# Kernel optimization log

Measured on AMD Instinct MI355X. Metric: run time of the kernel, lower is better.

## Reference

```python
import jax, jax.numpy as jnp
import numpy as np
from jax import lax

B, S, N, DIM = 4, 512, 16, 8
D_MODEL, D_STATE = 1024, 64
INPUT_SIZE = N * DIM
LN_EPS = 1e-5


def setup_inputs() -> dict:
    key = jax.random.key(0)
    ks = jax.random.split(key, 8)
    s = 0.02
    x = jax.random.normal(ks[0], (B, S, N, DIM), dtype=jnp.float32)
    W_emb = jax.random.normal(ks[1], (INPUT_SIZE, D_MODEL), dtype=jnp.float32) * s
    b_emb = jnp.zeros((D_MODEL,), jnp.float32)
    W_xp = jax.random.normal(ks[2], (D_MODEL, 2 * D_STATE + 1), dtype=jnp.float32) * s
    b_xp = jnp.zeros((2 * D_STATE + 1,), jnp.float32)
    # A init: -exp(arange(1, d_state+1) * 0.1), matching the torch module
    A = -jnp.exp(jnp.arange(1, D_STATE + 1, dtype=jnp.float32) * 0.1)
    Dp = jnp.ones((D_MODEL,), jnp.float32)
    gamma = jnp.ones((D_MODEL,), jnp.float32)
    beta = jnp.zeros((D_MODEL,), jnp.float32)
    W_out = jax.random.normal(ks[3], (D_MODEL, INPUT_SIZE), dtype=jnp.float32) * s
    b_out = jnp.zeros((INPUT_SIZE,), jnp.float32)
    return {"x": x, "W_emb": W_emb, "b_emb": b_emb, "W_xp": W_xp, "b_xp": b_xp,
            "A": A, "Dp": Dp, "gamma": gamma, "beta": beta,
            "W_out": W_out, "b_out": b_out}


def reference(x, W_emb, b_emb, W_xp, b_xp, A, Dp, gamma, beta, W_out, b_out):
    b, s, n, dim = x.shape
    d_state = A.shape[0]
    d_model = W_emb.shape[1]
    u = x.reshape(b, s, n * dim) @ W_emb + b_emb            # [B,S,dm]
    sel = u @ W_xp + b_xp                                    # [B,S,2*ds+1]
    delta = jax.nn.softplus(sel[..., 0:1]) * 0.01            # [B,S,1]
    Bs = sel[..., 1:1 + d_state]                             # [B,S,ds]
    Cs = sel[..., 1 + d_state:]                              # [B,S,ds]
    A_bar = jnp.exp(delta * A)                               # [B,S,ds]
    B_bar = delta * Bs                                       # [B,S,ds]

    def step(h, inp):
        a_t, b_t, c_t, u_t = inp                             # [B,ds],[B,ds],[B,ds],[B,dm]
        h = h * a_t[:, None, :] + b_t[:, None, :] * u_t[:, :, None]  # [B,dm,ds]
        y_t = jnp.einsum('bmd,bd->bm', h, c_t) + u_t * Dp
        return h, y_t

    h0 = jnp.zeros((b, d_model, d_state), x.dtype)
    xs = (jnp.swapaxes(A_bar, 0, 1), jnp.swapaxes(B_bar, 0, 1),
          jnp.swapaxes(Cs, 0, 1), jnp.swapaxes(u, 0, 1))
    _, ys = lax.scan(step, h0, xs)                           # ys: [S,B,dm]
    y = jnp.swapaxes(ys, 0, 1)                               # [B,S,dm]
    mu = y.mean(-1, keepdims=True)
    var = y.var(-1, keepdims=True)
    yn = (y - mu) / jnp.sqrt(var + LN_EPS) * gamma + beta
    pred = yn @ W_out + b_out                                # [B,S,N*D]
    return pred.reshape(b, s, n, dim)
```

## Files before the change

### kernel.cpp

```cpp
#include <hip/hip_runtime.h>
#include <cstddef>

typedef __attribute__((ext_vector_type(8))) short short8;
typedef __attribute__((ext_vector_type(4))) float f32x4;

constexpr int CL = 32;

__device__ inline ushort tobf(float f) {
  union { float f; unsigned u; } v; v.f = f;
  return (ushort)((v.u + 0x7FFFu + ((v.u >> 16) & 1u)) >> 16);
}
__device__ inline float frombf(ushort u) {
  union { unsigned u; float f; } v; v.u = ((unsigned)u) << 16; return v.f;
}

__global__ __launch_bounds__(256)
void prep(const float* __restrict__ Wemb, const float* __restrict__ Wxp,
          const float* __restrict__ Wout, const float* __restrict__ x,
          const float* __restrict__ bxp,
          ushort* __restrict__ WembT, ushort* __restrict__ wBCdT,
          ushort* __restrict__ WoutT, ushort* __restrict__ xbf,
          float* __restrict__ sel) {
  int idx = blockIdx.x * 256 + threadIdx.x;
  if (idx < 131072) {
    int n = idx >> 7, k = idx & 127;
    WembT[idx] = tobf(Wemb[k * 1024 + n]);
  } else if (idx < 327680) {
    int j = idx - 131072;
    int n = j >> 10, k = j & 1023;
    float v = (n < 128) ? Wxp[k * 129 + 1 + n] : (n == 128 ? Wxp[k * 129] : 0.f);
    wBCdT[j] = tobf(v);
  } else if (idx < 458752) {
    int j = idx - 327680;
    int n = j >> 10, k = j & 1023;
    WoutT[j] = tobf(Wout[k * 128 + n]);
  } else if (idx < 720896) {
    int j = idx - 458752;
    xbf[j] = tobf(x[j]);
  } else if (idx < 1114112) {
    int j = idx - 720896;
    int c = j % 192;
    sel[j] = (c < 128) ? bxp[1 + c] : (c == 128 ? bxp[0] : 0.f);
  }
}

template<int MODE>
__global__ __launch_bounds__(256)
void gemm_bt(const ushort* __restrict__ A, const ushort* __restrict__ BT,
             const float* __restrict__ bias, float* __restrict__ Cf,
             ushort* __restrict__ Cbf, int M, int N, int K, int kchunk) {
  __shared__ __align__(16) ushort sA[8192];
  __shared__ __align__(16) ushort sB[8192];
  const int t  = threadIdx.x;
  const int n0 = blockIdx.x * 64;
  const int m0 = blockIdx.y * 64;
  const int k0 = (MODE == 1) ? blockIdx.z * kchunk : 0;
  const int k1 = (MODE == 1) ? k0 + kchunk : K;

  const int lane = t & 63, w = t >> 6;
  const int wr = w << 4;
  const int colsel = lane & 15;
  const int kg = lane >> 4;

  f32x4 acc[4];
  #pragma unroll
  for (int nf = 0; nf < 4; ++nf) acc[nf] = (f32x4)(0.f);

  for (int kc = k0; kc < k1; kc += 128) {
    __syncthreads();
    #pragma unroll
    for (int i = 0; i < 4; ++i) {
      int c = t + (i << 8);
      int row = c >> 4, kk = (c & 15) << 3;
      float4 va  = *(const float4*)(A  + (size_t)(m0 + row) * K + kc + kk);
      float4 vb4 = *(const float4*)(BT + (size_t)(n0 + row) * K + kc + kk);
      int byteoff = ((row << 8) + (kk << 1)) ^ ((row & 7) << 4);
      *(float4*)((char*)sA + byteoff) = va;
      *(float4*)((char*)sB + byteoff) = vb4;
    }
    __syncthreads();
    short8 a[4];
    {
      int arow = wr + colsel;
      int lin = (arow << 8) + (kg << 4);
      int swz = (arow & 7) << 4;
      #pragma unroll
      for (int ks = 0; ks < 4; ++ks)
        a[ks] = *(const short8*)((const char*)sA + ((lin + (ks << 6)) ^ swz));
    }
    #pragma unroll
    for (int nf = 0; nf < 4; ++nf) {
      int brow = (nf << 4) + colsel;
      int lin = (brow << 8) + (kg << 4);
      int swz = (brow & 7) << 4;
      #pragma unroll
      for (int ks = 0; ks < 4; ++ks) {
        short8 b = *(const short8*)((const char*)sB + ((lin + (ks << 6)) ^ swz));
        acc[nf] = __builtin_amdgcn_mfma_f32_16x16x32_bf16(a[ks], b, acc[nf], 0, 0, 0);
      }
    }
  }
  const int r4 = kg << 2;
  #pragma unroll
  for (int nf = 0; nf < 4; ++nf) {
    int gn = n0 + (nf << 4) + colsel;
    #pragma unroll
    for (int reg = 0; reg < 4; ++reg) {
      int gm = m0 + wr + r4 + reg;
      if (MODE == 0) {
        Cbf[(size_t)gm * N + gn] = tobf(acc[nf][reg] + bias[gn]);
      } else {
        atomicAdd(&Cf[(size_t)gm * N + gn], acc[nf][reg]);
      }
    }
  }
}

__device__ __forceinline__ void transform_sbuf(float* sbuf, float a_d, int t) {
  const int d = t & 63;
  #pragma unroll
  for (int i = 0; i < 8; ++i) {
    float* R = sbuf + ((t >> 6) + i * 4) * 192;
    float draw = R[128];
    float sp = (draw > 15.f) ? draw : log1pf(__expf(draw));
    float delta = 0.01f * sp;
    R[d] = delta * R[d];
    R[128 + d] = __expf(delta * a_d);
  }
}

__global__ __launch_bounds__(256)
void scan_sum(const ushort* __restrict__ ubf, const float* __restrict__ sel,
              const float* __restrict__ A,
              float* __restrict__ cst, float* __restrict__ Ach) {
  __shared__ __align__(16) float sbuf[CL * 192];
  const int t = threadIdx.x, lane = t & 63, w = t >> 6;
  const int tc = blockIdx.x % 15;
  const int mg = (blockIdx.x / 15) & 3;
  const int b  = blockIdx.x / 60;
  const int r0 = b * 512 + tc * CL;

  const float a_d = A[t & 63];
  const float4* src = (const float4*)(sel + (size_t)r0 * 192);
  #pragma unroll
  for (int i = 0; i < 6; ++i)
    ((float4*)sbuf)[t + i * 256] = src[t + i * 256];
  __syncthreads();
  transform_sbuf(sbuf, a_d, t);
  __syncthreads();

  const int m = (mg * 4 + w) * 64 + lane;
  const ushort* ub = ubf + (size_t)r0 * 1024 + m;
  const bool doAp = (mg == 0 && w == 0);

  float2 h[32], ap[32];
  #pragma unroll
  for (int j = 0; j < 32; ++j) { h[j] = make_float2(0.f, 0.f); ap[j] = make_float2(1.f, 1.f); }

  float u0 = frombf(ub[0]);
  float u1 = frombf(ub[1024]);
  for (int s = 0; s < CL; ++s) {
    int sn = (s < CL - 3) ? s + 2 : CL - 1;
    float u2 = frombf(ub[(size_t)sn * 1024]);
    const float* L = sbuf + s * 192;
    #pragma unroll
    for (int jj = 0; jj < 16; ++jj) {
      float4 a4 = *(const float4*)&L[128 + 4 * jj];
      float4 b4 = *(const float4*)&L[4 * jj];
      h[2 * jj].x     = fmaf(h[2 * jj].x,     a4.x, b4.x * u0);
      h[2 * jj].y     = fmaf(h[2 * jj].y,     a4.y, b4.y * u0);
      h[2 * jj + 1].x = fmaf(h[2 * jj + 1].x, a4.z, b4.z * u0);
      h[2 * jj + 1].y = fmaf(h[2 * jj + 1].y, a4.w, b4.w * u0);
    }
    if (doAp) {
      #pragma unroll
      for (int jj = 0; jj < 16; ++jj) {
        float4 a4 = *(const float4*)&L[128 + 4 * jj];
        ap[2 * jj].x     *= a4.x;
        ap[2 * jj].y     *= a4.y;
        ap[2 * jj + 1].x *= a4.z;
        ap[2 * jj + 1].y *= a4.w;
      }
    }
    u0 = u1; u1 = u2;
  }

  size_t cbase = (((size_t)b * 15 + tc) * 64) * 1024 + m;
  #pragma unroll
  for (int j = 0; j < 32; ++j) {
    cst[cbase + (size_t)(2 * j)     * 1024] = h[j].x;
    cst[cbase + (size_t)(2 * j + 1) * 1024] = h[j].y;
  }
  if (doAp && lane == 0) {
    float2* ad = (float2*)&Ach[((size_t)b * 15 + tc) * 64];
    #pragma unroll
    for (int j = 0; j < 32; ++j) ad[j] = ap[j];
  }
}

__global__ __launch_bounds__(256)
void scan_comb(float* __restrict__ cst, const float* __restrict__ Ach) {
  int g = blockIdx.x * 256 + threadIdx.x;
  int b = g >> 16;
  int rem = g & 65535;
  int d = rem >> 10;
  int m = rem & 1023;
  float h = 0.f;
  for (int t2 = 0; t2 < 15; ++t2) {
    size_t idx = (((size_t)(b * 15 + t2)) * 64 + d) * 1024 + m;
    h = fmaf(Ach[(b * 15 + t2) * 64 + d], h, cst[idx]);
    cst[idx] = h;
  }
}

__global__ __launch_bounds__(256)
void scan_out(const ushort* __restrict__ ubf, const float* __restrict__ sel,
              const float* __restrict__ A, const float* __restrict__ cst,
              const float* __restrict__ Dp, float* __restrict__ y) {
  __shared__ __align__(16) float sbuf[CL * 192];
  const int t = threadIdx.x, lane = t & 63, w = t >> 6;
  const int tc = blockIdx.x & 15;
  const int mg = (blockIdx.x >> 4) & 3;
  const int b  = blockIdx.x >> 6;
  const int r0 = b * 512 + tc * CL;

  const float a_d = A[t & 63];
  const float4* src = (const float4*)(sel + (size_t)r0 * 192);
  #pragma unroll
  for (int i = 0; i < 6; ++i)
    ((float4*)sbuf)[t + i * 256] = src[t + i * 256];
  __syncthreads();
  transform_sbuf(sbuf, a_d, t);
  __syncthreads();

  const int m = (mg * 4 + w) * 64 + lane;
  const ushort* ub = ubf + (size_t)r0 * 1024 + m;
  float* yb = y + (size_t)r0 * 1024 + m;
  const float dp = Dp[m];

  float2 h[32];
  if (tc == 0) {
    #pragma unroll
    for (int j = 0; j < 32; ++j) h[j] = make_float2(0.f, 0.f);
  } else {
    size_t cbase = (((size_t)b * 15 + (tc - 1)) * 64) * 1024 + m;
    #pragma unroll
    for (int j = 0; j < 32; ++j) {
      h[j].x = cst[cbase + (size_t)(2 * j)     * 1024];
      h[j].y = cst[cbase + (size_t)(2 * j + 1) * 1024];
    }
  }

  float u0 = frombf(ub[0]);
  float u1 = frombf(ub[1024]);
  for (int s = 0; s < CL; ++s) {
    int sn = (s < CL - 3) ? s + 2 : CL - 1;
    float u2 = frombf(ub[(size_t)sn * 1024]);
    const float* L = sbuf + s * 192;
    float y0 = 0.f, y1 = 0.f, y2 = 0.f, y3 = 0.f;
    #pragma unroll
    for (int jj = 0; jj < 16; ++jj) {
      float4 a4 = *(const float4*)&L[128 + 4 * jj];
      float4 b4 = *(const float4*)&L[4 * jj];
      float4 c4 = *(const float4*)&L[64 + 4 * jj];
      h[2 * jj].x     = fmaf(h[2 * jj].x,     a4.x, b4.x * u0);
      h[2 * jj].y     = fmaf(h[2 * jj].y,     a4.y, b4.y * u0);
      h[2 * jj + 1].x = fmaf(h[2 * jj + 1].x, a4.z, b4.z * u0);
      h[2 * jj + 1].y = fmaf(h[2 * jj + 1].y, a4.w, b4.w * u0);
      y0 = fmaf(c4.x, h[2 * jj].x,     y0);
      y1 = fmaf(c4.y, h[2 * jj].y,     y1);
      y2 = fmaf(c4.z, h[2 * jj + 1].x, y2);
      y3 = fmaf(c4.w, h[2 * jj + 1].y, y3);
    }
    yb[(size_t)s * 1024] = (y0 + y1) + (y2 + y3) + u0 * dp;
    u0 = u1; u1 = u2;
  }
}

__global__ __launch_bounds__(256)
void k4a_ln(const float* __restrict__ y, const float* __restrict__ gamma,
            const float* __restrict__ beta, ushort* __restrict__ ynbf,
            const float* __restrict__ bout, float* __restrict__ out) {
  __shared__ float red[8];
  int t = threadIdx.x, lane = t & 63, wv = t >> 6;
  int gi = blockIdx.x * 256 + t;
  if (gi < 262144) out[gi] = bout[gi & 127];
  int row = blockIdx.x;
  float4 v = *(const float4*)&y[(size_t)row * 1024 + t * 4];
  float s1 = v.x + v.y + v.z + v.w;
  float s2 = v.x * v.x + v.y * v.y + v.z * v.z + v.w * v.w;
  #pragma unroll
  for (int o = 32; o; o >>= 1) {
    s1 += __shfl_xor(s1, o, 64);
    s2 += __shfl_xor(s2, o, 64);
  }
  if (lane == 0) { red[wv] = s1; red[4 + wv] = s2; }
  __syncthreads();
  float S1 = red[0] + red[1] + red[2] + red[3];
  float S2 = red[4] + red[5] + red[6] + red[7];
  float mean = S1 * (1.f / 1024.f);
  float var  = S2 * (1.f / 1024.f) - mean * mean;
  float rstd = rsqrtf(var + 1e-5f);
  float4 g  = *(const float4*)&gamma[t * 4];
  float4 be = *(const float4*)&beta[t * 4];
  ushort4 o4;
  o4.x = tobf((v.x - mean) * rstd * g.x + be.x);
  o4.y = tobf((v.y - mean) * rstd * g.y + be.y);
  o4.z = tobf((v.z - mean) * rstd * g.z + be.z);
  o4.w = tobf((v.w - mean) * rstd * g.w + be.w);
  *(ushort4*)&ynbf[(size_t)row * 1024 + t * 4] = o4;
}

extern "C" void kernel_launch(void* const* d_in, const int* in_sizes, int n_in,
                              void* d_out, int out_size, void* d_ws, size_t ws_size,
                              hipStream_t stream) {
  const float* x     = (const float*)d_in[0];
  const float* Wemb  = (const float*)d_in[1];
  const float* bemb  = (const float*)d_in[2];
  const float* Wxp   = (const float*)d_in[3];
  const float* bxp   = (const float*)d_in[4];
  const float* A     = (const float*)d_in[5];
  const float* Dp    = (const float*)d_in[6];
  const float* gamma = (const float*)d_in[7];
  const float* beta  = (const float*)d_in[8];
  const float* Wout  = (const float*)d_in[9];
  const float* bout  = (const float*)d_in[10];
  float* out = (float*)d_out;
  float* ws  = (float*)d_ws;

  float* sel = ws;
  float* cst = ws + 393216;
  float* y   = ws + 4325376;
  float* Ach = ws + 6422528;
  ushort* ubf   = (ushort*)(ws + 6426624);
  ushort* ynbf  = ubf + 2097152;
  ushort* xbf   = ynbf + 2097152;
  ushort* WembT = xbf + 262144;
  ushort* wBCdT = WembT + 131072;
  ushort* WoutT = wBCdT + 196608;

  prep<<<4352, 256, 0, stream>>>(Wemb, Wxp, Wout, x, bxp,
                                 WembT, wBCdT, WoutT, xbf, sel);
  gemm_bt<0><<<dim3(16, 32, 1), 256, 0, stream>>>(
      xbf, WembT, bemb, nullptr, ubf, 2048, 1024, 128, 0);
  gemm_bt<1><<<dim3(3, 32, 4), 256, 0, stream>>>(
      ubf, wBCdT, nullptr, sel, nullptr, 2048, 192, 1024, 256);
  scan_sum<<<240, 256, 0, stream>>>(ubf, sel, A, cst, Ach);
  scan_comb<<<1024, 256, 0, stream>>>(cst, Ach);
  scan_out<<<256, 256, 0, stream>>>(ubf, sel, A, cst, Dp, y);
  k4a_ln<<<2048, 256, 0, stream>>>(y, gamma, beta, ynbf, bout, out);
  gemm_bt<1><<<dim3(2, 32, 4), 256, 0, stream>>>(
      ynbf, WoutT, nullptr, out, nullptr, 2048, 128, 1024, 256);
}
```

Baseline: 160.8 us.

## Fuse LayerNorm stats into scan output and normalization into output GEMM

Removes the separate LayerNorm kernel. The scan now writes y as bf16 and accumulates per-row sum and sum-of-squares with wave shuffles plus atomics. The output GEMM computes mean and rstd from those sums and normalizes the A-tile while loading it into shared memory. Bias initialization of the output and zeroing of the sums buffer move into the prep kernel. This cuts one launch and the fp32 y round trip. In exchange it adds atomic contention in the scan loop, repeats the normalization for each N-block, and computes the statistics from fp32 values while the GEMM normalizes bf16-rounded y.

```diff
diff --git a/kernel.cpp b/kernel.cpp
--- a/kernel.cpp
+++ b/kernel.cpp
@@ -17,10 +17,11 @@
 __global__ __launch_bounds__(256)
 void prep(const float* __restrict__ Wemb, const float* __restrict__ Wxp,
           const float* __restrict__ Wout, const float* __restrict__ x,
-          const float* __restrict__ bxp,
+          const float* __restrict__ bxp, const float* __restrict__ bout,
           ushort* __restrict__ WembT, ushort* __restrict__ wBCdT,
           ushort* __restrict__ WoutT, ushort* __restrict__ xbf,
-          float* __restrict__ sel) {
+          float* __restrict__ sel, float* __restrict__ sums,
+          float* __restrict__ out) {
   int idx = blockIdx.x * 256 + threadIdx.x;
   if (idx < 131072) {
     int n = idx >> 7, k = idx & 127;
@@ -41,6 +42,11 @@
     int j = idx - 720896;
     int c = j % 192;
     sel[j] = (c < 128) ? bxp[1 + c] : (c == 128 ? bxp[0] : 0.f);
+  } else if (idx < 1118208) {
+    sums[idx - 1114112] = 0.f;
+  } else if (idx < 1380352) {
+    int j = idx - 1118208;
+    out[j] = bout[j & 127];
   }
 }
 
@@ -112,6 +118,96 @@
       } else {
         atomicAdd(&Cf[(size_t)gm * N + gn], acc[nf][reg]);
       }
+    }
+  }
+}
+
+__global__ __launch_bounds__(256)
+void gemm_ln(const ushort* __restrict__ ybf, const ushort* __restrict__ BT,
+             const float* __restrict__ sums, const float* __restrict__ gamma,
+             const float* __restrict__ beta, float* __restrict__ out) {
+  __shared__ __align__(16) ushort sA[8192];
+  __shared__ __align__(16) ushort sB[8192];
+  __shared__ float sLN[128];
+  const int t  = threadIdx.x;
+  const int n0 = blockIdx.x * 64;
+  const int m0 = blockIdx.y * 64;
+  const int k0 = blockIdx.z * 256;
+  const int k1 = k0 + 256;
+
+  if (t < 64) {
+    float s1 = sums[m0 + t], s2 = sums[2048 + m0 + t];
+    float mean = s1 * (1.f / 1024.f);
+    float var  = s2 * (1.f / 1024.f) - mean * mean;
+    sLN[2 * t] = mean;
+    sLN[2 * t + 1] = rsqrtf(var + 1e-5f);
+  }
+
+  const int lane = t & 63, w = t >> 6;
+  const int wr = w << 4;
+  const int colsel = lane & 15;
+  const int kg = lane >> 4;
+  const int kk_t = (t & 15) << 3;
+
+  f32x4 acc[4];
+  #pragma unroll
+  for (int nf = 0; nf < 4; ++nf) acc[nf] = (f32x4)(0.f);
+
+  for (int kc = k0; kc < k1; kc += 128) {
+    float4 g0 = *(const float4*)&gamma[kc + kk_t];
+    float4 g1 = *(const float4*)&gamma[kc + kk_t + 4];
+    float4 be0 = *(const float4*)&beta[kc + kk_t];
+    float4 be1 = *(const float4*)&beta[kc + kk_t + 4];
+    float gv[8] = {g0.x, g0.y, g0.z, g0.w, g1.x, g1.y, g1.z, g1.w};
+    float bv[8] = {be0.x, be0.y, be0.z, be0.w, be1.x, be1.y, be1.z, be1.w};
+    __syncthreads();
+    #pragma unroll
+    for (int i = 0; i < 4; ++i) {
+      int c = t + (i << 8);
+      int row = c >> 4, kk = (c & 15) << 3;
+      short8 ya = *(const short8*)(ybf + (size_t)(m0 + row) * 1024 + kc + kk);
+      float4 vb4 = *(const float4*)(BT + (size_t)(n0 + row) * 1024 + kc + kk);
+      float mean = sLN[2 * row], rstd = sLN[2 * row + 1];
+      short8 na;
+      #pragma unroll
+      for (int j = 0; j < 8; ++j) {
+        float yv = frombf((ushort)ya[j]);
+        na[j] = (short)tobf((yv - mean) * rstd * gv[j] + bv[j]);
+      }
+      int byteoff = ((row << 8) + (kk << 1)) ^ ((row & 7) << 4);
+      *(short8*)((char*)sA + byteoff) = na;
+      *(float4*)((char*)sB + byteoff) = vb4;
+    }
+    __syncthreads();
+    short8 a[4];
+    {
+      int arow = wr + colsel;
+      int lin = (arow << 8) + (kg << 4);
+      int swz = (arow & 7) << 4;
+      #pragma unroll
+      for (int ks = 0; ks < 4; ++ks)
+        a[ks] = *(const short8*)((const char*)sA + ((lin + (ks << 6)) ^ swz));
+    }
+    #pragma unroll
+    for (int nf = 0; nf < 4; ++nf) {
+      int brow = (nf << 4) + colsel;
+      int lin = (brow << 8) + (kg << 4);
+      int swz = (brow & 7) << 4;
+      #pragma unroll
+      for (int ks = 0; ks < 4; ++ks) {
+        short8 b = *(const short8*)((const char*)sB + ((lin + (ks << 6)) ^ swz));
+        acc[nf] = __builtin_amdgcn_mfma_f32_16x16x32_bf16(a[ks], b, acc[nf], 0, 0, 0);
+      }
+    }
+  }
+  const int r4 = kg << 2;
+  #pragma unroll
+  for (int nf = 0; nf < 4; ++nf) {
+    int gn = n0 + (nf << 4) + colsel;
+    #pragma unroll
+    for (int reg = 0; reg < 4; ++reg) {
+      int gm = m0 + wr + r4 + reg;
+      atomicAdd(&out[(size_t)gm * 128 + gn], acc[nf][reg]);
     }
   }
 }
@@ -216,7 +312,8 @@
 __global__ __launch_bounds__(256)
 void scan_out(const ushort* __restrict__ ubf, const float* __restrict__ sel,
               const float* __restrict__ A, const float* __restrict__ cst,
-              const float* __restrict__ Dp, float* __restrict__ y) {
+              const float* __restrict__ Dp, ushort* __restrict__ ybf,
+              float* __restrict__ sums) {
   __shared__ __align__(16) float sbuf[CL * 192];
   const int t = threadIdx.x, lane = t & 63, w = t >> 6;
   const int tc = blockIdx.x & 15;
@@ -235,7 +332,7 @@
 
   const int m = (mg * 4 + w) * 64 + lane;
   const ushort* ub = ubf + (size_t)r0 * 1024 + m;
-  float* yb = y + (size_t)r0 * 1024 + m;
+  ushort* yb = ybf + (size_t)r0 * 1024 + m;
   const float dp = Dp[m];
 
   float2 h[32];
@@ -272,43 +369,20 @@
       y2 = fmaf(c4.z, h[2 * jj + 1].x, y2);
       y3 = fmaf(c4.w, h[2 * jj + 1].y, y3);
     }
-    yb[(size_t)s * 1024] = (y0 + y1) + (y2 + y3) + u0 * dp;
+    float yv = (y0 + y1) + (y2 + y3) + u0 * dp;
+    yb[(size_t)s * 1024] = tobf(yv);
+    float rs1 = yv, rs2 = yv * yv;
+    #pragma unroll
+    for (int o = 32; o; o >>= 1) {
+      rs1 += __shfl_xor(rs1, o, 64);
+      rs2 += __shfl_xor(rs2, o, 64);
+    }
+    if (lane == 0) {
+      atomicAdd(&sums[r0 + s], rs1);
+      atomicAdd(&sums[2048 + r0 + s], rs2);
+    }
     u0 = u1; u1 = u2;
   }
-}
-
-__global__ __launch_bounds__(256)
-void k4a_ln(const float* __restrict__ y, const float* __restrict__ gamma,
-            const float* __restrict__ beta, ushort* __restrict__ ynbf,
-            const float* __restrict__ bout, float* __restrict__ out) {
-  __shared__ float red[8];
-  int t = threadIdx.x, lane = t & 63, wv = t >> 6;
-  int gi = blockIdx.x * 256 + t;
-  if (gi < 262144) out[gi] = bout[gi & 127];
-  int row = blockIdx.x;
-  float4 v = *(const float4*)&y[(size_t)row * 1024 + t * 4];
-  float s1 = v.x + v.y + v.z + v.w;
-  float s2 = v.x * v.x + v.y * v.y + v.z * v.z + v.w * v.w;
-  #pragma unroll
-  for (int o = 32; o; o >>= 1) {
-    s1 += __shfl_xor(s1, o, 64);
-    s2 += __shfl_xor(s2, o, 64);
-  }
-  if (lane == 0) { red[wv] = s1; red[4 + wv] = s2; }
-  __syncthreads();
-  float S1 = red[0] + red[1] + red[2] + red[3];
-  float S2 = red[4] + red[5] + red[6] + red[7];
-  float mean = S1 * (1.f / 1024.f);
-  float var  = S2 * (1.f / 1024.f) - mean * mean;
-  float rstd = rsqrtf(var + 1e-5f);
-  float4 g  = *(const float4*)&gamma[t * 4];
-  float4 be = *(const float4*)&beta[t * 4];
-  ushort4 o4;
-  o4.x = tobf((v.x - mean) * rstd * g.x + be.x);
-  o4.y = tobf((v.y - mean) * rstd * g.y + be.y);
-  o4.z = tobf((v.z - mean) * rstd * g.z + be.z);
-  o4.w = tobf((v.w - mean) * rstd * g.w + be.w);
-  *(ushort4*)&ynbf[(size_t)row * 1024 + t * 4] = o4;
 }
 
 extern "C" void kernel_launch(void* const* d_in, const int* in_sizes, int n_in,
@@ -328,27 +402,26 @@
   float* out = (float*)d_out;
   float* ws  = (float*)d_ws;
 
-  float* sel = ws;
-  float* cst = ws + 393216;
-  float* y   = ws + 4325376;
-  float* Ach = ws + 6422528;
-  ushort* ubf   = (ushort*)(ws + 6426624);
-  ushort* ynbf  = ubf + 2097152;
-  ushort* xbf   = ynbf + 2097152;
+  float* sel  = ws;
+  float* cst  = ws + 393216;
+  float* Ach  = ws + 4325376;
+  float* sums = ws + 4329472;
+  ushort* ubf   = (ushort*)(ws + 4333568);
+  ushort* ybf   = ubf + 2097152;
+  ushort* xbf   = ybf + 2097152;
   ushort* WembT = xbf + 262144;
   ushort* wBCdT = WembT + 131072;
   ushort* WoutT = wBCdT + 196608;
 
-  prep<<<4352, 256, 0, stream>>>(Wemb, Wxp, Wout, x, bxp,
-                                 WembT, wBCdT, WoutT, xbf, sel);
+  prep<<<5392, 256, 0, stream>>>(Wemb, Wxp, Wout, x, bxp, bout,
+                                 WembT, wBCdT, WoutT, xbf, sel, sums, out);
   gemm_bt<0><<<dim3(16, 32, 1), 256, 0, stream>>>(
       xbf, WembT, bemb, nullptr, ubf, 2048, 1024, 128, 0);
   gemm_bt<1><<<dim3(3, 32, 4), 256, 0, stream>>>(
       ubf, wBCdT, nullptr, sel, nullptr, 2048, 192, 1024, 256);
   scan_sum<<<240, 256, 0, stream>>>(ubf, sel, A, cst, Ach);
   scan_comb<<<1024, 256, 0, stream>>>(cst, Ach);
-  scan_out<<<256, 256, 0, stream>>>(ubf, sel, A, cst, Dp, y);
-  k4a_ln<<<2048, 256, 0, stream>>>(y, gamma, beta, ynbf, bout, out);
-  gemm_bt<1><<<dim3(2, 32, 4), 256, 0, stream>>>(
-      ynbf, WoutT, nullptr, out, nullptr, 2048, 128, 1024, 256);
-}
+  scan_out<<<256, 256, 0, stream>>>(ubf, sel, A, cst, Dp, ybf, sums);
+  gemm_ln<<<dim3(2, 32, 4), 256, 0, stream>>>(
+      ybf, WoutT, sums, gamma, beta, out);
+}
```

Result: slower. 186.3 us (+15.9%).
